# Kernel tuning notes

Measured on AMD Instinct MI355X. Metric: run time of the kernel, lower is better.

The kernel has to match this reference:

```python
import jax, jax.numpy as jnp
import numpy as np

EMBED_DIM = 1024
CONTEXT_DIM = 768
NUM_HEADS = 16
HEAD_DIM = EMBED_DIM // NUM_HEADS
B, N, M = 8, 4096, 77


def setup_inputs() -> dict:
    key = jax.random.key(0)
    ks = jax.random.split(key, 12)
    s_in = 1.0 / np.sqrt(EMBED_DIM)
    s_ctx = 1.0 / np.sqrt(CONTEXT_DIM)
    x = jax.random.normal(ks[0], (B, N, EMBED_DIM), dtype=jnp.float32)
    context = jax.random.normal(ks[1], (B, M, CONTEXT_DIM), dtype=jnp.float32)
    # realistic padding mask: each example has a random valid prefix length in [1, M]
    lengths = jax.random.randint(ks[2], (B,), 1, M + 1)
    context_mask = jnp.arange(M)[None, :] < lengths[:, None]  # (B, M) bool
    Wq = jax.random.uniform(ks[3], (EMBED_DIM, EMBED_DIM), jnp.float32, -s_in, s_in)
    bq = jax.random.uniform(ks[4], (EMBED_DIM,), jnp.float32, -s_in, s_in)
    Wk = jax.random.uniform(ks[5], (CONTEXT_DIM, EMBED_DIM), jnp.float32, -s_ctx, s_ctx)
    bk = jax.random.uniform(ks[6], (EMBED_DIM,), jnp.float32, -s_ctx, s_ctx)
    Wv = jax.random.uniform(ks[7], (CONTEXT_DIM, EMBED_DIM), jnp.float32, -s_ctx, s_ctx)
    bv = jax.random.uniform(ks[8], (EMBED_DIM,), jnp.float32, -s_ctx, s_ctx)
    Wo = jax.random.uniform(ks[9], (EMBED_DIM, EMBED_DIM), jnp.float32, -s_in, s_in)
    bo = jax.random.uniform(ks[10], (EMBED_DIM,), jnp.float32, -s_in, s_in)
    return {"x": x, "context": context, "context_mask": context_mask,
            "Wq": Wq, "bq": bq, "Wk": Wk, "bk": bk, "Wv": Wv, "bv": bv,
            "Wo": Wo, "bo": bo}


def reference(x, context, context_mask, Wq, bq, Wk, bk, Wv, bv, Wo, bo):
    H, d = NUM_HEADS, HEAD_DIM
    scale = d ** -0.5
    Bx, Nx, _ = x.shape
    Mx = context.shape[1]
    # projections
    q = (x @ Wq + bq).reshape(Bx, Nx, H, d).transpose(0, 2, 1, 3)        # (B,H,N,d)
    k = (context @ Wk + bk).reshape(Bx, Mx, H, d).transpose(0, 2, 1, 3)  # (B,H,M,d)
    v = (context @ Wv + bv).reshape(Bx, Mx, H, d).transpose(0, 2, 1, 3)  # (B,H,M,d)
    # scores with padding mask
    attn = jnp.einsum('bhnd,bhmd->bhnm', q, k) * scale                   # (B,H,N,M)
    attn = jnp.where(context_mask[:, None, None, :], attn, -jnp.inf)
    attn = jax.nn.softmax(attn, axis=-1)
    out = jnp.einsum('bhnm,bhmd->bhnd', attn, v)                          # (B,H,N,d)
    out = out.transpose(0, 2, 1, 3).reshape(Bx, Nx, H * d)                # (B,N,E)
    return out @ Wo + bo
```

## Files before the change

kernel.cpp:

```cpp
#include <hip/hip_runtime.h>

typedef __bf16 bf16x8 __attribute__((ext_vector_type(8)));
typedef float f32x4 __attribute__((ext_vector_type(4)));

#define EMB 1024
#define CTXD 768
#define NH 16
#define HD 64
#define BB 8
#define NN 4096
#define MM 77
#define MPAD 96

static __device__ __forceinline__ unsigned short f2bf(float f) {
    unsigned u = __builtin_bit_cast(unsigned, f);
    u += 0x7FFFu + ((u >> 16) & 1u);
    return (unsigned short)(u >> 16);
}

__global__ void mask_lengths_kernel(const unsigned char* __restrict__ mask,
                                    int* __restrict__ lengths) {
    int ln = threadIdx.x & 63;
    int anyOdd = 0, anyF = 0;
    for (int i = ln; i < BB * MM; i += 64) {
        unsigned char v = mask[i];
        if (v == 0x80u || v == 0x3Fu) anyF = 1;
        if ((i & 3) && v) anyOdd = 1;
    }
    anyF = __any(anyF); anyOdd = __any(anyOdd);
    int layout = anyF ? 2 : (anyOdd ? 1 : 0);
    int b = ln >> 3, j = ln & 7, cnt = 0;
    for (int m = j; m < MM; m += 8) {
        int idx = b * MM + m;
        int valid;
        if (layout == 1)      valid = mask[idx] != 0;
        else if (layout == 0) valid = ((const int*)mask)[idx] != 0;
        else                  valid = ((const float*)mask)[idx] != 0.0f;
        cnt += valid ? 1 : 0;
    }
    cnt += __shfl_xor(cnt, 1, 64);
    cnt += __shfl_xor(cnt, 2, 64);
    cnt += __shfl_xor(cnt, 4, 64);
    if (j == 0) lengths[b] = cnt;
}

__global__ void cast_f32_to_bf16(const float* __restrict__ in,
                                 unsigned short* __restrict__ out, int n8) {
    for (int i = blockIdx.x * blockDim.x + threadIdx.x; i < n8;
         i += gridDim.x * blockDim.x) {
        float4 v0 = ((const float4*)in)[2 * i];
        float4 v1 = ((const float4*)in)[2 * i + 1];
        union { unsigned short u[8]; int4 v; } r;
        r.u[0] = f2bf(v0.x); r.u[1] = f2bf(v0.y);
        r.u[2] = f2bf(v0.z); r.u[3] = f2bf(v0.w);
        r.u[4] = f2bf(v1.x); r.u[5] = f2bf(v1.y);
        r.u[6] = f2bf(v1.z); r.u[7] = f2bf(v1.w);
        ((int4*)out)[i] = r.v;
    }
}

__global__ void cast_ctx_kernel(const float* __restrict__ in,
                                unsigned short* __restrict__ out) {
    int i = blockIdx.x * 256 + threadIdx.x;
    if (i >= 640 * CTXD / 8) return;
    int row = (i * 8) / CTXD;
    union { unsigned short u[8]; int4 v; } r;
    if (row < BB * MM) {
        float4 v0 = ((const float4*)in)[2 * i];
        float4 v1 = ((const float4*)in)[2 * i + 1];
        r.u[0] = f2bf(v0.x); r.u[1] = f2bf(v0.y);
        r.u[2] = f2bf(v0.z); r.u[3] = f2bf(v0.w);
        r.u[4] = f2bf(v1.x); r.u[5] = f2bf(v1.y);
        r.u[6] = f2bf(v1.z); r.u[7] = f2bf(v1.w);
    } else {
        r.v = make_int4(0, 0, 0, 0);
    }
    ((int4*)out)[i] = r.v;
}

struct TPtrs { const float* src[4]; unsigned short* dst[4]; };
__global__ void transpose4_kernel(TPtrs tp) {
    __shared__ float t[32][33];
    int z = blockIdx.z;
    int R = (z < 2) ? 1024 : 768, C = 1024;
    int r0 = blockIdx.y * 32;
    if (r0 >= R) return;
    const float* W = tp.src[z];
    unsigned short* Wt = tp.dst[z];
    int tx = threadIdx.x, ty = threadIdx.y;
    int c0 = blockIdx.x * 32;
#pragma unroll
    for (int i = 0; i < 32; i += 8)
        t[ty + i][tx] = W[(size_t)(r0 + ty + i) * C + c0 + tx];
    __syncthreads();
#pragma unroll
    for (int i = 0; i < 32; i += 8)
        Wt[(size_t)(c0 + ty + i) * R + r0 + tx] = f2bf(t[tx][ty + i]);
}

template <int MODE>
__global__ __launch_bounds__(512, 2) void gemm256_kernel(
    const unsigned short* __restrict__ A, const unsigned short* __restrict__ Bt,
    const float* __restrict__ bias, void* __restrict__ Cout,
    int M, int N, int K) {
    __shared__ unsigned short lds[4][2][256 * 32];
    const int tid = threadIdx.x, wv = tid >> 6, ln = tid & 63;
    const int numN = N >> 8;
    int bid = blockIdx.x;
    const int nwg = (M >> 8) * numN;
    if ((nwg & 7) == 0) { int cpx = nwg >> 3; bid = (bid & 7) * cpx + (bid >> 3); }
    const int nt_ = bid % numN, mt = bid / numN;
    const int m0 = mt << 8, n0 = nt_ << 8;
    const int wr = wv >> 2, wc = wv & 3;
    const int NT = K >> 5;

    const int srow = wv * 16 + (ln >> 2);
    const int sslot = ln & 3;

    auto stageA = [&](int t) {
#pragma unroll
        for (int half = 0; half < 2; ++half) {
            int row = half * 128 + srow;
            int gc = sslot ^ ((row >> 1) & 3);
            __builtin_amdgcn_global_load_lds(
                (const __attribute__((address_space(1))) void*)(
                    A + (size_t)(m0 + row) * K + (t << 5) + gc * 8),
                (__attribute__((address_space(3))) void*)(
                    &lds[t & 3][0][(half * 128 + wv * 16) * 32]),
                16, 0, 0);
        }
    };
    auto stageB = [&](int t) {
#pragma unroll
        for (int half = 0; half < 2; ++half) {
            int row = half * 128 + srow;
            int gc = sslot ^ ((row >> 1) & 3);
            __builtin_amdgcn_global_load_lds(
                (const __attribute__((address_space(1))) void*)(
                    Bt + (size_t)(n0 + row) * K + (t << 5) + gc * 8),
                (__attribute__((address_space(3))) void*)(
                    &lds[t & 3][1][(half * 128 + wv * 16) * 32]),
                16, 0, 0);
        }
    };
    auto readA = [&](const unsigned short* As, int i) -> bf16x8 {
        int arow = wr * 128 + i * 16 + (ln & 15);
        int aslot = (ln >> 4) ^ ((arow >> 1) & 3);
        return *(const bf16x8*)(As + arow * 32 + aslot * 8);
    };
    auto readB = [&](const unsigned short* Bs, int j) -> bf16x8 {
        int brow = wc * 64 + j * 16 + (ln & 15);
        int bslot = (ln >> 4) ^ ((brow >> 1) & 3);
        return *(const bf16x8*)(Bs + brow * 32 + bslot * 8);
    };

    f32x4 acc[8][4] = {};
    bf16x8 afA[4], afB[4], bfrC[4], afN[4], bfrN[4];

    stageA(0); stageB(0); stageA(1); stageB(1); stageA(2); stageB(2);
    asm volatile("s_waitcnt vmcnt(4)" ::: "memory");
    __builtin_amdgcn_sched_barrier(0);
    __builtin_amdgcn_s_barrier();
#pragma unroll
    for (int i = 0; i < 4; ++i) afA[i] = readA(lds[0][0], i);
#pragma unroll
    for (int j = 0; j < 4; ++j) bfrC[j] = readB(lds[0][1], j);

#pragma unroll 4
    for (int t = 0; t < NT; ++t) {
        const unsigned short* As = lds[t & 3][0];
        const unsigned short* Asn = lds[(t + 1) & 3][0];
        const unsigned short* Bsn = lds[(t + 1) & 3][1];
        if (t + 3 < NT) stageA(t + 3);
#pragma unroll
        for (int i = 0; i < 4; ++i) afB[i] = readA(As, i + 4);
        __builtin_amdgcn_s_barrier();
        __builtin_amdgcn_s_setprio(1);
#pragma unroll
        for (int i = 0; i < 4; ++i)
#pragma unroll
            for (int j = 0; j < 4; ++j)
                acc[i][j] = __builtin_amdgcn_mfma_f32_16x16x32_bf16(
                    afA[i], bfrC[j], acc[i][j], 0, 0, 0);
        __builtin_amdgcn_s_setprio(0);
        __builtin_amdgcn_s_barrier();
        if (t + 3 < NT) stageB(t + 3);
        if (t + 1 < NT) {
#pragma unroll
            for (int i = 0; i < 4; ++i) afN[i] = readA(Asn, i);
#pragma unroll
            for (int j = 0; j < 4; ++j) bfrN[j] = readB(Bsn, j);
        }
        if (t + 3 < NT) { asm volatile("s_waitcnt vmcnt(4)" ::: "memory"); }
        else            { asm volatile("s_waitcnt vmcnt(0)" ::: "memory"); }
        __builtin_amdgcn_sched_barrier(0);
        __builtin_amdgcn_s_barrier();
        __builtin_amdgcn_s_setprio(1);
#pragma unroll
        for (int i = 0; i < 4; ++i)
#pragma unroll
            for (int j = 0; j < 4; ++j)
                acc[i + 4][j] = __builtin_amdgcn_mfma_f32_16x16x32_bf16(
                    afB[i], bfrC[j], acc[i + 4][j], 0, 0, 0);
        __builtin_amdgcn_s_setprio(0);
        __builtin_amdgcn_s_barrier();
#pragma unroll
        for (int i = 0; i < 4; ++i) afA[i] = afN[i];
#pragma unroll
        for (int j = 0; j < 4; ++j) bfrC[j] = bfrN[j];
    }

    float bvals[4];
#pragma unroll
    for (int j = 0; j < 4; ++j)
        bvals[j] = bias[n0 + wc * 64 + j * 16 + (ln & 15)];
#pragma unroll
    for (int i = 0; i < 8; ++i)
#pragma unroll
        for (int j = 0; j < 4; ++j)
#pragma unroll
            for (int r = 0; r < 4; ++r) {
                int row = m0 + wr * 128 + i * 16 + (ln >> 4) * 4 + r;
                int col = n0 + wc * 64 + j * 16 + (ln & 15);
                float v = acc[i][j][r] + bvals[j];
                if constexpr (MODE == 0)
                    ((unsigned short*)Cout)[(size_t)row * N + col] = f2bf(v);
                else
                    ((float*)Cout)[(size_t)row * N + col] = v;
            }
}

static __device__ __forceinline__ void stage_tile(
    const unsigned short* __restrict__ G, int ldg, unsigned short* lds,
    int r0, int kt, int wv, int ln) {
    int rown = ln >> 2;
    int koff = (ln & 3) * 8;
#pragma unroll
    for (int r = 0; r < 2; ++r) {
        int cw = wv * 2 + r;
        const unsigned short* src =
            G + (size_t)(r0 + cw * 16 + rown) * ldg + kt + koff;
        __builtin_amdgcn_global_load_lds(
            (const __attribute__((address_space(1))) void*)src,
            (__attribute__((address_space(3))) void*)(lds + cw * 512),
            16, 0, 0);
    }
}

template <int MODE>
__global__ __launch_bounds__(256) void gemm_bt_kernel(
    const unsigned short* __restrict__ A, const unsigned short* __restrict__ Bt,
    const float* __restrict__ bias, void* __restrict__ Cout,
    int M, int N, int K) {
    __shared__ unsigned short As[128 * 32];
    __shared__ unsigned short Bs[128 * 32];
    const int tid = threadIdx.x, wv = tid >> 6, ln = tid & 63;
    const int numM = M >> 7, numN = N >> 7;
    int bid = blockIdx.x;
    const int nwg = numM * numN;
    if ((nwg & 7) == 0) { int cpx = nwg >> 3; bid = (bid & 7) * cpx + (bid >> 3); }
    const int nt = bid % numN, mt = bid / numN;
    const int m0 = mt << 7, n0 = nt << 7;
    const int wr = wv >> 1, wc = wv & 1;

    f32x4 acc[4][4] = {};
    for (int kt = 0; kt < K; kt += 32) {
        __syncthreads();
        stage_tile(A, K, As, m0, kt, wv, ln);
        stage_tile(Bt, K, Bs, n0, kt, wv, ln);
        __syncthreads();
        bf16x8 af[4], bfr[4];
#pragma unroll
        for (int i = 0; i < 4; ++i)
            af[i] = *(const bf16x8*)(As + (wr * 64 + i * 16 + (ln & 15)) * 32 +
                                     (ln >> 4) * 8);
#pragma unroll
        for (int j = 0; j < 4; ++j)
            bfr[j] = *(const bf16x8*)(Bs + (wc * 64 + j * 16 + (ln & 15)) * 32 +
                                      (ln >> 4) * 8);
#pragma unroll
        for (int i = 0; i < 4; ++i)
#pragma unroll
            for (int j = 0; j < 4; ++j)
                acc[i][j] = __builtin_amdgcn_mfma_f32_16x16x32_bf16(
                    af[i], bfr[j], acc[i][j], 0, 0, 0);
    }

    float bvals[4];
#pragma unroll
    for (int j = 0; j < 4; ++j)
        bvals[j] = bias[n0 + wc * 64 + j * 16 + (ln & 15)];

#pragma unroll
    for (int i = 0; i < 4; ++i) {
#pragma unroll
        for (int j = 0; j < 4; ++j) {
#pragma unroll
            for (int r = 0; r < 4; ++r) {
                int row = m0 + wr * 64 + i * 16 + (ln >> 4) * 4 + r;
                int col = n0 + wc * 64 + j * 16 + (ln & 15);
                float v = acc[i][j][r] + bvals[j];
                if (row < BB * MM) {
                    int bb = row / MM, m = row - bb * MM;
                    int hh = col >> 6, d = col & 63;
                    if constexpr (MODE == 2)
                        ((unsigned short*)Cout)[((size_t)(bb * NH + hh) * MPAD + m) * HD + d] = f2bf(v);
                    else
                        ((unsigned short*)Cout)[((size_t)(bb * NH + hh) * HD + d) * MPAD + m] = f2bf(v);
                }
            }
        }
    }
}

__global__ __launch_bounds__(256, 3) void attn_kernel(
    const unsigned short* __restrict__ Q, const unsigned short* __restrict__ Kw,
    const unsigned short* __restrict__ Vt, const int* __restrict__ lengths,
    unsigned short* __restrict__ Out) {
    const int bh = blockIdx.y;
    const int b = bh >> 4, h = bh & 15;
    const int q0 = blockIdx.x * 128;
    const int tid = threadIdx.x, wv = tid >> 6, ln = tid & 63;
    const int len = lengths[b];
    const int kscnt = (len + 31) >> 5;

    __shared__ unsigned short Ps[128][104];

    const unsigned short* Ksrc = Kw + (size_t)bh * (MPAD * HD);
    const unsigned short* Vsrc = Vt + (size_t)bh * (HD * MPAD);

    bf16x8 aq[2][2];
#pragma unroll
    for (int qi = 0; qi < 2; ++qi) {
        const int qr = q0 + wv * 32 + qi * 16 + (ln & 15);
        const unsigned short* qptr =
            Q + (size_t)(b * NN + qr) * EMB + h * HD + (ln >> 4) * 8;
        aq[qi][0] = *(const bf16x8*)(qptr);
        aq[qi][1] = *(const bf16x8*)(qptr + 32);
    }

    bf16x8 vf[3][4];
#pragma unroll
    for (int j = 0; j < 4; ++j)
        vf[0][j] = *(const bf16x8*)(Vsrc + (j * 16 + (ln & 15)) * MPAD +
                                    (ln >> 4) * 8);
    if (kscnt > 1) {
#pragma unroll
        for (int j = 0; j < 4; ++j)
            vf[1][j] = *(const bf16x8*)(Vsrc + (j * 16 + (ln & 15)) * MPAD + 32 +
                                        (ln >> 4) * 8);
    }
    if (kscnt > 2) {
#pragma unroll
        for (int j = 0; j < 4; ++j)
            vf[2][j] = *(const bf16x8*)(Vsrc + (j * 16 + (ln & 15)) * MPAD + 64 +
                                        (ln >> 4) * 8);
    }

    f32x4 s[2][5] = {};
#pragma unroll
    for (int t = 0; t < 5; ++t) {
        if (t * 16 < len) {
            const unsigned short* kp =
                Ksrc + (t * 16 + (ln & 15)) * HD + (ln >> 4) * 8;
            bf16x8 k0 = *(const bf16x8*)(kp);
            bf16x8 k1 = *(const bf16x8*)(kp + 32);
#pragma unroll
            for (int qi = 0; qi < 2; ++qi) {
                s[qi][t] = __builtin_amdgcn_mfma_f32_16x16x32_bf16(
                    aq[qi][0], k0, s[qi][t], 0, 0, 0);
                s[qi][t] = __builtin_amdgcn_mfma_f32_16x16x32_bf16(
                    aq[qi][1], k1, s[qi][t], 0, 0, 0);
            }
        }
    }

    const float scale = 0.125f;
    float mx[2][4], sum[2][4];
#pragma unroll
    for (int qi = 0; qi < 2; ++qi)
#pragma unroll
        for (int r = 0; r < 4; ++r) { mx[qi][r] = -1e30f; sum[qi][r] = 0.f; }
#pragma unroll
    for (int t = 0; t < 5; ++t) {
        int m = t * 16 + (ln & 15);
        bool valid = m < len;
#pragma unroll
        for (int qi = 0; qi < 2; ++qi)
#pragma unroll
            for (int r = 0; r < 4; ++r) {
                float v = valid ? s[qi][t][r] * scale : -1e30f;
                s[qi][t][r] = v;
                mx[qi][r] = fmaxf(mx[qi][r], v);
            }
    }
#pragma unroll
    for (int d = 1; d < 16; d <<= 1)
#pragma unroll
        for (int qi = 0; qi < 2; ++qi)
#pragma unroll
            for (int r = 0; r < 4; ++r)
                mx[qi][r] = fmaxf(mx[qi][r], __shfl_xor(mx[qi][r], d, 64));
#pragma unroll
    for (int t = 0; t < 5; ++t)
#pragma unroll
        for (int qi = 0; qi < 2; ++qi)
#pragma unroll
            for (int r = 0; r < 4; ++r) {
                float p = __expf(s[qi][t][r] - mx[qi][r]);
                s[qi][t][r] = p;
                sum[qi][r] += p;
            }
#pragma unroll
    for (int d = 1; d < 16; d <<= 1)
#pragma unroll
        for (int qi = 0; qi < 2; ++qi)
#pragma unroll
            for (int r = 0; r < 4; ++r)
                sum[qi][r] += __shfl_xor(sum[qi][r], d, 64);

    float rinv[2][4];
#pragma unroll
    for (int qi = 0; qi < 2; ++qi)
#pragma unroll
        for (int r = 0; r < 4; ++r) rinv[qi][r] = 1.0f / sum[qi][r];

#pragma unroll
    for (int t = 0; t < 6; ++t)
#pragma unroll
        for (int qi = 0; qi < 2; ++qi)
#pragma unroll
            for (int r = 0; r < 4; ++r) {
                int row = wv * 32 + qi * 16 + (ln >> 4) * 4 + r;
                float v = (t < 5) ? s[qi][t][r] * rinv[qi][r] : 0.0f;
                Ps[row][t * 16 + (ln & 15)] = f2bf(v);
            }

    f32x4 o[2][4] = {};
    for (int ks = 0; ks < kscnt; ++ks) {
#pragma unroll
        for (int qi = 0; qi < 2; ++qi) {
            bf16x8 pf = *(const bf16x8*)(&Ps[wv * 32 + qi * 16 + (ln & 15)]
                                            [ks * 32 + (ln >> 4) * 8]);
#pragma unroll
            for (int j = 0; j < 4; ++j)
                o[qi][j] = __builtin_amdgcn_mfma_f32_16x16x32_bf16(
                    vf[ks][j], pf, o[qi][j], 0, 0, 0);
        }
    }

#pragma unroll
    for (int qi = 0; qi < 2; ++qi) {
        const int qrow = q0 + wv * 32 + qi * 16 + (ln & 15);
        unsigned short* obase =
            Out + (size_t)(b * NN + qrow) * EMB + h * HD + (ln >> 4) * 4;
#pragma unroll
        for (int j = 0; j < 4; ++j) {
            union { unsigned short u[4]; unsigned long long ll; } pk;
#pragma unroll
            for (int r = 0; r < 4; ++r) pk.u[r] = f2bf(o[qi][j][r]);
            *(unsigned long long*)(obase + j * 16) = pk.ll;
        }
    }
}

extern "C" void kernel_launch(void* const* d_in, const int* in_sizes, int n_in,
                              void* d_out, int out_size, void* d_ws, size_t ws_size,
                              hipStream_t stream) {
    const float* x    = (const float*)d_in[0];
    const float* ctx  = (const float*)d_in[1];
    const unsigned char* cmask = (const unsigned char*)d_in[2];
    const float* Wq = (const float*)d_in[3];
    const float* bq = (const float*)d_in[4];
    const float* Wk = (const float*)d_in[5];
    const float* bk = (const float*)d_in[6];
    const float* Wv = (const float*)d_in[7];
    const float* bv = (const float*)d_in[8];
    const float* Wo = (const float*)d_in[9];
    const float* bo = (const float*)d_in[10];

    char* ws = (char*)d_ws;
    unsigned short* Xbf   = (unsigned short*)(ws);
    unsigned short* Wq_t  = (unsigned short*)(ws + 67108864);
    unsigned short* Wo_t  = (unsigned short*)(ws + 69206016);
    unsigned short* Wk_t  = (unsigned short*)(ws + 71303168);
    unsigned short* Wv_t  = (unsigned short*)(ws + 72876032);
    unsigned short* Cbf   = (unsigned short*)(ws + 74448896);
    unsigned short* Kw    = (unsigned short*)(ws + 75431936);
    unsigned short* Vtw   = (unsigned short*)(ws + 77004800);
    int* lengths          = (int*)(ws + 78577664);
    unsigned short* Qb    = (unsigned short*)d_out;

    mask_lengths_kernel<<<1, 64, 0, stream>>>(cmask, lengths);
    cast_f32_to_bf16<<<2048, 256, 0, stream>>>(x, Xbf, (BB * NN * EMB) / 8);
    cast_ctx_kernel<<<240, 256, 0, stream>>>(ctx, Cbf);
    TPtrs tp;
    tp.src[0] = Wq; tp.src[1] = Wo; tp.src[2] = Wk; tp.src[3] = Wv;
    tp.dst[0] = Wq_t; tp.dst[1] = Wo_t; tp.dst[2] = Wk_t; tp.dst[3] = Wv_t;
    transpose4_kernel<<<dim3(32, 32, 4), dim3(32, 8), 0, stream>>>(tp);
    hipMemsetAsync(Kw, 0, 2 * 1572864, stream);

    gemm256_kernel<0><<<512, 512, 0, stream>>>(Xbf, Wq_t, bq, Qb, 32768, 1024, 1024);
    gemm_bt_kernel<2><<<40, 256, 0, stream>>>(Cbf, Wk_t, bk, Kw, 640, 1024, 768);
    gemm_bt_kernel<3><<<40, 256, 0, stream>>>(Cbf, Wv_t, bv, Vtw, 640, 1024, 768);

    attn_kernel<<<dim3(32, 128), 256, 0, stream>>>(Qb, Kw, Vtw, lengths, Xbf);

    gemm256_kernel<1><<<512, 512, 0, stream>>>(Xbf, Wo_t, bo, d_out, 32768, 1024, 1024);
}
```

Measured before the change: 326.5 us.

## Merge prep kernels and KV GEMMs, simplify GEMM256 LDS prefetch schedule

Merges the mask-length, context cast, weight transposes and K/V buffer zeroing into a single prep launch, and combines the K and V projection GEMMs into one 80-block launch, cutting launch count and the small per-launch gaps between them. Separately, the main 256x256 GEMM loop drops the register double-buffering of the next tile's LDS fragments and instead reads the current tile's fragments at the start of each iteration, with relaxed vmcnt waits (8/4/0). This lowers register pressure but exposes LDS read latency before the MFMAs, which may hurt the two large GEMMs that dominate runtime.

```diff
diff --git a/kernel.cpp b/kernel.cpp
--- a/kernel.cpp
+++ b/kernel.cpp
@@ -16,32 +16,6 @@
     unsigned u = __builtin_bit_cast(unsigned, f);
     u += 0x7FFFu + ((u >> 16) & 1u);
     return (unsigned short)(u >> 16);
-}
-
-__global__ void mask_lengths_kernel(const unsigned char* __restrict__ mask,
-                                    int* __restrict__ lengths) {
-    int ln = threadIdx.x & 63;
-    int anyOdd = 0, anyF = 0;
-    for (int i = ln; i < BB * MM; i += 64) {
-        unsigned char v = mask[i];
-        if (v == 0x80u || v == 0x3Fu) anyF = 1;
-        if ((i & 3) && v) anyOdd = 1;
-    }
-    anyF = __any(anyF); anyOdd = __any(anyOdd);
-    int layout = anyF ? 2 : (anyOdd ? 1 : 0);
-    int b = ln >> 3, j = ln & 7, cnt = 0;
-    for (int m = j; m < MM; m += 8) {
-        int idx = b * MM + m;
-        int valid;
-        if (layout == 1)      valid = mask[idx] != 0;
-        else if (layout == 0) valid = ((const int*)mask)[idx] != 0;
-        else                  valid = ((const float*)mask)[idx] != 0.0f;
-        cnt += valid ? 1 : 0;
-    }
-    cnt += __shfl_xor(cnt, 1, 64);
-    cnt += __shfl_xor(cnt, 2, 64);
-    cnt += __shfl_xor(cnt, 4, 64);
-    if (j == 0) lengths[b] = cnt;
 }
 
 __global__ void cast_f32_to_bf16(const float* __restrict__ in,
@@ -59,43 +33,80 @@
     }
 }
 
-__global__ void cast_ctx_kernel(const float* __restrict__ in,
-                                unsigned short* __restrict__ out) {
-    int i = blockIdx.x * 256 + threadIdx.x;
-    if (i >= 640 * CTXD / 8) return;
-    int row = (i * 8) / CTXD;
-    union { unsigned short u[8]; int4 v; } r;
-    if (row < BB * MM) {
-        float4 v0 = ((const float4*)in)[2 * i];
-        float4 v1 = ((const float4*)in)[2 * i + 1];
-        r.u[0] = f2bf(v0.x); r.u[1] = f2bf(v0.y);
-        r.u[2] = f2bf(v0.z); r.u[3] = f2bf(v0.w);
-        r.u[4] = f2bf(v1.x); r.u[5] = f2bf(v1.y);
-        r.u[6] = f2bf(v1.z); r.u[7] = f2bf(v1.w);
+struct PrepArgs {
+    const float* wsrc[4];
+    unsigned short* wdst[4];
+    const float* ctx;
+    unsigned short* cbf;
+    const unsigned char* mask;
+    int* lengths;
+    int4* kvzero;
+};
+__global__ void prep_kernel(PrepArgs pa) {
+    const int z = blockIdx.z;
+    const int tx = threadIdx.x, ty = threadIdx.y;
+    const int tid = ty * 32 + tx;
+    if (z < 4) {
+        __shared__ float t[32][33];
+        int R = (z < 2) ? 1024 : 768, C = 1024;
+        int r0 = blockIdx.y * 32;
+        if (r0 >= R) return;
+        const float* W = pa.wsrc[z];
+        unsigned short* Wt = pa.wdst[z];
+        int c0 = blockIdx.x * 32;
+#pragma unroll
+        for (int i = 0; i < 32; i += 8)
+            t[ty + i][tx] = W[(size_t)(r0 + ty + i) * C + c0 + tx];
+        __syncthreads();
+#pragma unroll
+        for (int i = 0; i < 32; i += 8)
+            Wt[(size_t)(c0 + ty + i) * R + r0 + tx] = f2bf(t[tx][ty + i]);
+    } else if (z == 4) {
+        int fid = blockIdx.y * 32 + blockIdx.x;
+        int i = fid * 256 + tid;
+        if (i >= 640 * CTXD / 8) return;
+        int row = (i * 8) / CTXD;
+        union { unsigned short u[8]; int4 v; } r;
+        if (row < BB * MM) {
+            float4 v0 = ((const float4*)pa.ctx)[2 * i];
+            float4 v1 = ((const float4*)pa.ctx)[2 * i + 1];
+            r.u[0] = f2bf(v0.x); r.u[1] = f2bf(v0.y);
+            r.u[2] = f2bf(v0.z); r.u[3] = f2bf(v0.w);
+            r.u[4] = f2bf(v1.x); r.u[5] = f2bf(v1.y);
+            r.u[6] = f2bf(v1.z); r.u[7] = f2bf(v1.w);
+        } else {
+            r.v = make_int4(0, 0, 0, 0);
+        }
+        ((int4*)pa.cbf)[i] = r.v;
     } else {
-        r.v = make_int4(0, 0, 0, 0);
-    }
-    ((int4*)out)[i] = r.v;
-}
-
-struct TPtrs { const float* src[4]; unsigned short* dst[4]; };
-__global__ void transpose4_kernel(TPtrs tp) {
-    __shared__ float t[32][33];
-    int z = blockIdx.z;
-    int R = (z < 2) ? 1024 : 768, C = 1024;
-    int r0 = blockIdx.y * 32;
-    if (r0 >= R) return;
-    const float* W = tp.src[z];
-    unsigned short* Wt = tp.dst[z];
-    int tx = threadIdx.x, ty = threadIdx.y;
-    int c0 = blockIdx.x * 32;
-#pragma unroll
-    for (int i = 0; i < 32; i += 8)
-        t[ty + i][tx] = W[(size_t)(r0 + ty + i) * C + c0 + tx];
-    __syncthreads();
-#pragma unroll
-    for (int i = 0; i < 32; i += 8)
-        Wt[(size_t)(c0 + ty + i) * R + r0 + tx] = f2bf(t[tx][ty + i]);
+        int fid = blockIdx.y * 32 + blockIdx.x;
+        int i = fid * 256 + tid;
+        if (i < 196608) pa.kvzero[i] = make_int4(0, 0, 0, 0);
+        if (fid == 1023 && tid < 64) {
+            int ln = tid;
+            int anyOdd = 0, anyF = 0;
+            for (int k = ln; k < BB * MM; k += 64) {
+                unsigned char v = pa.mask[k];
+                if (v == 0x80u || v == 0x3Fu) anyF = 1;
+                if ((k & 3) && v) anyOdd = 1;
+            }
+            anyF = __any(anyF); anyOdd = __any(anyOdd);
+            int layout = anyF ? 2 : (anyOdd ? 1 : 0);
+            int b = ln >> 3, j = ln & 7, cnt = 0;
+            for (int m = j; m < MM; m += 8) {
+                int idx = b * MM + m;
+                int valid;
+                if (layout == 1)      valid = pa.mask[idx] != 0;
+                else if (layout == 0) valid = ((const int*)pa.mask)[idx] != 0;
+                else                  valid = ((const float*)pa.mask)[idx] != 0.0f;
+                cnt += valid ? 1 : 0;
+            }
+            cnt += __shfl_xor(cnt, 1, 64);
+            cnt += __shfl_xor(cnt, 2, 64);
+            cnt += __shfl_xor(cnt, 4, 64);
+            if (j == 0) pa.lengths[b] = cnt;
+        }
+    }
 }
 
 template <int MODE>
@@ -155,25 +166,22 @@
     };
 
     f32x4 acc[8][4] = {};
-    bf16x8 afA[4], afB[4], bfrC[4], afN[4], bfrN[4];
 
     stageA(0); stageB(0); stageA(1); stageB(1); stageA(2); stageB(2);
-    asm volatile("s_waitcnt vmcnt(4)" ::: "memory");
+    asm volatile("s_waitcnt vmcnt(8)" ::: "memory");
     __builtin_amdgcn_sched_barrier(0);
     __builtin_amdgcn_s_barrier();
-#pragma unroll
-    for (int i = 0; i < 4; ++i) afA[i] = readA(lds[0][0], i);
-#pragma unroll
-    for (int j = 0; j < 4; ++j) bfrC[j] = readB(lds[0][1], j);
 
 #pragma unroll 4
     for (int t = 0; t < NT; ++t) {
         const unsigned short* As = lds[t & 3][0];
-        const unsigned short* Asn = lds[(t + 1) & 3][0];
-        const unsigned short* Bsn = lds[(t + 1) & 3][1];
+        const unsigned short* Bs = lds[t & 3][1];
         if (t + 3 < NT) stageA(t + 3);
-#pragma unroll
-        for (int i = 0; i < 4; ++i) afB[i] = readA(As, i + 4);
+        bf16x8 bfr[4], af[4];
+#pragma unroll
+        for (int j = 0; j < 4; ++j) bfr[j] = readB(Bs, j);
+#pragma unroll
+        for (int i = 0; i < 4; ++i) af[i] = readA(As, i);
         __builtin_amdgcn_s_barrier();
         __builtin_amdgcn_s_setprio(1);
 #pragma unroll
@@ -181,19 +189,12 @@
 #pragma unroll
             for (int j = 0; j < 4; ++j)
                 acc[i][j] = __builtin_amdgcn_mfma_f32_16x16x32_bf16(
-                    afA[i], bfrC[j], acc[i][j], 0, 0, 0);
+                    af[i], bfr[j], acc[i][j], 0, 0, 0);
         __builtin_amdgcn_s_setprio(0);
         __builtin_amdgcn_s_barrier();
         if (t + 3 < NT) stageB(t + 3);
-        if (t + 1 < NT) {
-#pragma unroll
-            for (int i = 0; i < 4; ++i) afN[i] = readA(Asn, i);
-#pragma unroll
-            for (int j = 0; j < 4; ++j) bfrN[j] = readB(Bsn, j);
-        }
-        if (t + 3 < NT) { asm volatile("s_waitcnt vmcnt(4)" ::: "memory"); }
-        else            { asm volatile("s_waitcnt vmcnt(0)" ::: "memory"); }
-        __builtin_amdgcn_sched_barrier(0);
+#pragma unroll
+        for (int i = 0; i < 4; ++i) af[i] = readA(As, i + 4);
         __builtin_amdgcn_s_barrier();
         __builtin_amdgcn_s_setprio(1);
 #pragma unroll
@@ -201,13 +202,15 @@
 #pragma unroll
             for (int j = 0; j < 4; ++j)
                 acc[i + 4][j] = __builtin_amdgcn_mfma_f32_16x16x32_bf16(
-                    afB[i], bfrC[j], acc[i + 4][j], 0, 0, 0);
+                    af[i], bfr[j], acc[i + 4][j], 0, 0, 0);
         __builtin_amdgcn_s_setprio(0);
+        if (t < NT - 1) {
+            if (t + 3 < NT)      { asm volatile("s_waitcnt vmcnt(8)" ::: "memory"); }
+            else if (t + 2 < NT) { asm volatile("s_waitcnt vmcnt(4)" ::: "memory"); }
+            else                 { asm volatile("s_waitcnt vmcnt(0)" ::: "memory"); }
+            __builtin_amdgcn_sched_barrier(0);
+        }
         __builtin_amdgcn_s_barrier();
-#pragma unroll
-        for (int i = 0; i < 4; ++i) afA[i] = afN[i];
-#pragma unroll
-        for (int j = 0; j < 4; ++j) bfrC[j] = bfrN[j];
     }
 
     float bvals[4];
@@ -247,18 +250,23 @@
     }
 }
 
-template <int MODE>
-__global__ __launch_bounds__(256) void gemm_bt_kernel(
-    const unsigned short* __restrict__ A, const unsigned short* __restrict__ Bt,
-    const float* __restrict__ bias, void* __restrict__ Cout,
-    int M, int N, int K) {
+__global__ __launch_bounds__(256) void gemm_kv_kernel(
+    const unsigned short* __restrict__ Cbf,
+    const unsigned short* __restrict__ Wk_t, const float* __restrict__ bk,
+    unsigned short* __restrict__ Kw,
+    const unsigned short* __restrict__ Wv_t, const float* __restrict__ bv,
+    unsigned short* __restrict__ Vtw) {
+    const int M = 640, N = 1024, K = CTXD;
     __shared__ unsigned short As[128 * 32];
     __shared__ unsigned short Bs[128 * 32];
     const int tid = threadIdx.x, wv = tid >> 6, ln = tid & 63;
-    const int numM = M >> 7, numN = N >> 7;
     int bid = blockIdx.x;
-    const int nwg = numM * numN;
-    if ((nwg & 7) == 0) { int cpx = nwg >> 3; bid = (bid & 7) * cpx + (bid >> 3); }
+    const bool isV = bid >= 40;
+    if (isV) bid -= 40;
+    const unsigned short* Bt = isV ? Wv_t : Wk_t;
+    const float* bias = isV ? bv : bk;
+    const int numN = N >> 7;
+    { int cpx = 5; bid = (bid & 7) * cpx + (bid >> 3); }
     const int nt = bid % numN, mt = bid / numN;
     const int m0 = mt << 7, n0 = nt << 7;
     const int wr = wv >> 1, wc = wv & 1;
@@ -266,7 +274,7 @@
     f32x4 acc[4][4] = {};
     for (int kt = 0; kt < K; kt += 32) {
         __syncthreads();
-        stage_tile(A, K, As, m0, kt, wv, ln);
+        stage_tile(Cbf, K, As, m0, kt, wv, ln);
         stage_tile(Bt, K, Bs, n0, kt, wv, ln);
         __syncthreads();
         bf16x8 af[4], bfr[4];
@@ -303,10 +311,10 @@
                 if (row < BB * MM) {
                     int bb = row / MM, m = row - bb * MM;
                     int hh = col >> 6, d = col & 63;
-                    if constexpr (MODE == 2)
-                        ((unsigned short*)Cout)[((size_t)(bb * NH + hh) * MPAD + m) * HD + d] = f2bf(v);
+                    if (!isV)
+                        Kw[((size_t)(bb * NH + hh) * MPAD + m) * HD + d] = f2bf(v);
                     else
-                        ((unsigned short*)Cout)[((size_t)(bb * NH + hh) * HD + d) * MPAD + m] = f2bf(v);
+                        Vtw[((size_t)(bb * NH + hh) * HD + d) * MPAD + m] = f2bf(v);
                 }
             }
         }
@@ -491,18 +499,17 @@
     int* lengths          = (int*)(ws + 78577664);
     unsigned short* Qb    = (unsigned short*)d_out;
 
-    mask_lengths_kernel<<<1, 64, 0, stream>>>(cmask, lengths);
+    PrepArgs pa;
+    pa.wsrc[0] = Wq; pa.wsrc[1] = Wo; pa.wsrc[2] = Wk; pa.wsrc[3] = Wv;
+    pa.wdst[0] = Wq_t; pa.wdst[1] = Wo_t; pa.wdst[2] = Wk_t; pa.wdst[3] = Wv_t;
+    pa.ctx = ctx; pa.cbf = Cbf; pa.mask = cmask; pa.lengths = lengths;
+    pa.kvzero = (int4*)Kw;
+    prep_kernel<<<dim3(32, 32, 6), dim3(32, 8), 0, stream>>>(pa);
+
     cast_f32_to_bf16<<<2048, 256, 0, stream>>>(x, Xbf, (BB * NN * EMB) / 8);
-    cast_ctx_kernel<<<240, 256, 0, stream>>>(ctx, Cbf);
-    TPtrs tp;
-    tp.src[0] = Wq; tp.src[1] = Wo; tp.src[2] = Wk; tp.src[3] = Wv;
-    tp.dst[0] = Wq_t; tp.dst[1] = Wo_t; tp.dst[2] = Wk_t; tp.dst[3] = Wv_t;
-    transpose4_kernel<<<dim3(32, 32, 4), dim3(32, 8), 0, stream>>>(tp);
-    hipMemsetAsync(Kw, 0, 2 * 1572864, stream);
 
     gemm256_kernel<0><<<512, 512, 0, stream>>>(Xbf, Wq_t, bq, Qb, 32768, 1024, 1024);
-    gemm_bt_kernel<2><<<40, 256, 0, stream>>>(Cbf, Wk_t, bk, Kw, 640, 1024, 768);
-    gemm_bt_kernel<3><<<40, 256, 0, stream>>>(Cbf, Wv_t, bv, Vtw, 640, 1024, 768);
+    gemm_kv_kernel<<<80, 256, 0, stream>>>(Cbf, Wk_t, bk, Kw, Wv_t, bv, Vtw);
 
     attn_kernel<<<dim3(32, 128), 256, 0, stream>>>(Qb, Kw, Vtw, lengths, Xbf);
 
```

New measurement: 293.5 us. 10.1% less time.
